# Optimization experiments

Measured on AMD Instinct MI355X. Metric: run time of the kernel, lower is better.

The kernel has to match this reference:

```python
import jax, jax.numpy as jnp
import numpy as np

N, D, DFF, E, F, K, H = 4096, 512, 512, 512, 4096, 1024, 4


def _rn(i, shape, s=0.02):
    return jax.random.normal(jax.random.fold_in(jax.random.key(0), i), shape, dtype=jnp.float32) * s


def setup_inputs():
    inp = {"inputs": jax.random.normal(jax.random.key(1), (N, D), dtype=jnp.float32)}
    i = 10
    for p in ("enc", "dec"):
        for nm, shp in (("wq", (D, D)), ("wk", (D, D)), ("wv", (D, D)), ("wo", (D, D)), ("w1", (D, DFF)), ("w2", (DFF, D))):
            inp[p + "_" + nm] = _rn(i, shp); i += 1
        for nm, shp in (("bq", (D,)), ("bk", (D,)), ("bv", (D,)), ("bo", (D,)), ("b1", (DFF,)), ("b2", (D,))):
            inp[p + "_" + nm] = jnp.zeros(shp, jnp.float32)
        inp[p + "_ln1_g"] = jnp.ones((D,), jnp.float32)
        inp[p + "_ln1_b"] = jnp.zeros((D,), jnp.float32)
        inp[p + "_ln2_g"] = jnp.ones((D,), jnp.float32)
        inp[p + "_ln2_b"] = jnp.zeros((D,), jnp.float32)
    inp["fc1_w"] = _rn(100, (D, E))
    inp["fc1_b"] = jnp.zeros((E,), jnp.float32)
    inp["fc2_w"] = _rn(101, (D, F))
    inp["fc2_b"] = jnp.zeros((F,), jnp.float32)
    inp["emb"] = _rn(102, (K, E), s=0.01)
    return inp


def layer_norm(x, g, b, eps=1e-6):
    mu = jnp.mean(x, axis=-1, keepdims=True)
    var = jnp.mean(jnp.square(x - mu), axis=-1, keepdims=True)
    return (x - mu) * jax.lax.rsqrt(var + eps) * g + b


def row_distance(a, b):
    # cosine similarity between rows (sim in [-1,1]; loss maps (sim+1)/2 -> [0,1])
    an = a * jax.lax.rsqrt(jnp.maximum(jnp.sum(a * a, axis=1, keepdims=True), 1e-12))
    bn = b * jax.lax.rsqrt(jnp.maximum(jnp.sum(b * b, axis=1, keepdims=True), 1e-12))
    return an @ bn.T


def nearest_context(feature, context):
    distances = row_distance(feature, context) * -1.0  # [N, K]
    min_ind = jnp.argmin(distances, axis=1)
    one_hot = jax.nn.one_hot(min_ind, context.shape[0], dtype=jnp.float32)  # [N, K]
    rslt = one_hot @ jax.lax.stop_gradient(context)  # [N, E]
    return rslt, one_hot


@jax.custom_vjp
def vq(feature, context):
    return nearest_context(feature, context)[0]


def _vq_fwd(feature, context):
    value, ind = nearest_context(feature, context)
    return value, ind


def _vq_bwd(ind, d_value):
    # straight-through to feature, scatter-add (via one-hot matmul) to codebook
    return d_value, ind.T @ d_value


vq.defvjp(_vq_fwd, _vq_bwd)


def encoder_layer(x, wq, bq, wk, bk, wv, bv, wo, bo, w1, b1, w2, b2, g1, be1, g2, be2):
    n, d = x.shape
    dh = d // H
    q = (x @ wq + bq).reshape(n, H, dh)
    k = (x @ wk + bk).reshape(n, H, dh)
    v = (x @ wv + bv).reshape(n, H, dh)
    scores = jnp.einsum('nhd,mhd->hnm', q, k) / jnp.sqrt(jnp.float32(dh))
    attn = jax.nn.softmax(scores, axis=-1)
    ctx = jnp.einsum('hnm,mhd->nhd', attn, v).reshape(n, d)
    out1 = layer_norm(x + (ctx @ wo + bo), g1, be1)
    ffn = jax.nn.relu(out1 @ w1 + b1) @ w2 + b2
    return layer_norm(out1 + ffn, g2, be2)


def reference(inputs, enc_wq, enc_wk, enc_wv, enc_wo, enc_w1, enc_w2, enc_bq, enc_bk, enc_bv, enc_bo, enc_b1, enc_b2, enc_ln1_g, enc_ln1_b, enc_ln2_g, enc_ln2_b, dec_wq, dec_wk, dec_wv, dec_wo, dec_w1, dec_w2, dec_bq, dec_bk, dec_bv, dec_bo, dec_b1, dec_b2, dec_ln1_g, dec_ln1_b, dec_ln2_g, dec_ln2_b, fc1_w, fc1_b, fc2_w, fc2_b, emb):
    encoded = encoder_layer(inputs, enc_wq, enc_bq, enc_wk, enc_bk, enc_wv, enc_bv, enc_wo, enc_bo, enc_w1, enc_b1, enc_w2, enc_b2, enc_ln1_g, enc_ln1_b, enc_ln2_g, enc_ln2_b)
    encoded = encoded @ fc1_w + fc1_b  # [N, E]
    vq_feat = vq(encoded, emb)
    _, context_ind = nearest_context(encoded, emb)
    decoded = encoder_layer(vq_feat, dec_wq, dec_bq, dec_wk, dec_bk, dec_wv, dec_bv, dec_wo, dec_bo, dec_w1, dec_b1, dec_w2, dec_b2, dec_ln1_g, dec_ln1_b, dec_ln2_g, dec_ln2_b)
    decoded = jax.nn.relu(decoded @ fc2_w + fc2_b)  # [N, F]
    return encoded, vq_feat, context_ind, decoded, emb
```

## Files before the change

kernel.cpp:

```cpp
#include <hip/hip_runtime.h>
#include <hip/hip_bf16.h>
#include <stdint.h>

typedef __bf16 bf16;
typedef __bf16 bf16x8 __attribute__((ext_vector_type(8)));
typedef float  f32x4v __attribute__((ext_vector_type(4)));

__device__ __forceinline__ void cvt8(const float* v, bf16x8& hh, bf16x8& ll) {
    #pragma unroll
    for (int j = 0; j < 8; j++) {
        bf16 b = (bf16)v[j]; hh[j] = b; ll[j] = (bf16)(v[j] - (float)b);
    }
}

__device__ __forceinline__ float block_reduce_sum256(float v) {
    __shared__ float red[256];
    int tid = threadIdx.x;
    red[tid] = v; __syncthreads();
    #pragma unroll
    for (int s = 128; s > 0; s >>= 1) {
        if (tid < s) red[tid] += red[tid + s];
        __syncthreads();
    }
    float r = red[0]; __syncthreads();
// ... 110 lines not shown
}

template<int BMT, bool RELU>
__global__ __launch_bounds__(256, 2)
void gemm3p(const float* __restrict__ A,
            const bf16* __restrict__ Bph, const bf16* __restrict__ Bpl,
            const float* __restrict__ bias, float* __restrict__ C,
            int K, int lda, int ldb, int ldc)
{
    constexpr int BN = 128, TK = 32;
    constexpr int RM = BMT / 32;
    __shared__ __align__(16) bf16 Ah[BMT * TK];
    __shared__ __align__(16) bf16 Al[BMT * TK];
    __shared__ __align__(16) bf16 Bh[BN * TK];
    __shared__ __align__(16) bf16 Bl[BN * TK];

    const int tid  = threadIdx.x;
    const int wave = tid >> 6, lane = tid & 63;
    const int wr = wave >> 1, wc = wave & 1;
    const long bm = (long)blockIdx.y * BMT;
    const long bn = (long)blockIdx.x * BN;
    const int fr = lane & 15, fq = lane >> 4;

    f32x4v acc[RM][4] = {};

    for (int k0 = 0; k0 < K; k0 += TK) {
        #pragma unroll
        for (int it = 0; it < BMT / 64; it++) {
            const int c = it * 256 + tid;
            const int r = c >> 2, k8 = c & 3;
            const float* src = A + (bm + r) * (long)lda + k0 + k8 * 8;
            float4 f0 = ((const float4*)src)[0], f1 = ((const float4*)src)[1];
            float v[8] = {f0.x, f0.y, f0.z, f0.w, f1.x, f1.y, f1.z, f1.w};
            bf16x8 hh, ll; cvt8(v, hh, ll);
            *(bf16x8*)&Ah[r * TK + k8 * 8] = hh;
            *(bf16x8*)&Al[r * TK + k8 * 8] = ll;
        }
        #pragma unroll
        for (int it = 0; it < 2; it++) {
            const int c = it * 256 + tid;
            const int r = c >> 2, k8 = c & 3;
            const long bo = (bn + r) * (long)ldb + k0 + k8 * 8;
            *(uint4*)&Bh[r * TK + k8 * 8] = *(const uint4*)&Bph[bo];
            *(uint4*)&Bl[r * TK + k8 * 8] = *(const uint4*)&Bpl[bo];
        }
        __syncthreads();

        bf16x8 ah[RM], am[RM], bh[4], bm_[4];
        #pragma unroll
        for (int i = 0; i < RM; i++) {
            const int r = (wr * (BMT / 2) + i * 16 + fr) * TK + fq * 8;
            ah[i] = *(const bf16x8*)&Ah[r];
            am[i] = *(const bf16x8*)&Al[r];
        }
        #pragma unroll
        for (int j = 0; j < 4; j++) {
            const int r = (wc * 64 + j * 16 + fr) * TK + fq * 8;
            bh[j] = *(const bf16x8*)&Bh[r];
            bm_[j] = *(const bf16x8*)&Bl[r];
        }
        #pragma unroll
        for (int i = 0; i < RM; i++)
            #pragma unroll
            for (int j = 0; j < 4; j++) {
                acc[i][j] = __builtin_amdgcn_mfma_f32_16x16x32_bf16(am[i], bh[j], acc[i][j], 0, 0, 0);
                acc[i][j] = __builtin_amdgcn_mfma_f32_16x16x32_bf16(ah[i], bm_[j], acc[i][j], 0, 0, 0);
                acc[i][j] = __builtin_amdgcn_mfma_f32_16x16x32_bf16(ah[i], bh[j], acc[i][j], 0, 0, 0);
            }
        __syncthreads();
    }

    #pragma unroll
    for (int i = 0; i < RM; i++) {
        #pragma unroll
        for (int j = 0; j < 4; j++) {
            const long col = bn + wc * 64 + j * 16 + fr;
            const float bv = bias ? bias[col] : 0.f;
            #pragma unroll
            for (int r = 0; r < 4; r++) {
                const long row = bm + wr * (BMT / 2) + i * 16 + fq * 4 + r;
                float v = acc[i][j][r] + bv;
                if (RELU) v = fmaxf(v, 0.f);
                C[row * (long)ldc + col] = v;
            }
        }
    }
}

__global__ __launch_bounds__(256, 2)
void qkv_gemm(const float* __restrict__ X,
              const float* __restrict__ Wq, const float* __restrict__ Wk, const float* __restrict__ Wv,
              const float* __restrict__ Bq, const float* __restrict__ Bk, const float* __restrict__ Bv,
              float* __restrict__ Qo, bf16* __restrict__ Khi, bf16* __restrict__ Klo,
              bf16* __restrict__ Vthi, bf16* __restrict__ Vtlo)
{
    constexpr int TK = 32, D = 512, N = 4096;
    __shared__ __align__(16) bf16 Ah[64 * TK];
    __shared__ __align__(16) bf16 Al[64 * TK];
    __shared__ __align__(16) bf16 Bh[128 * TK];
    __shared__ __align__(16) bf16 Bl[128 * TK];

    const int tid  = threadIdx.x;
    const int wave = tid >> 6, lane = tid & 63;
    const int wr = wave >> 1, wc = wave & 1;
    const int sel = blockIdx.x >> 2, wcol0 = (blockIdx.x & 3) * 128;
    const long bm = (long)blockIdx.y * 64;
    const int fr = lane & 15, fq = lane >> 4;

    const float* W  = sel == 0 ? Wq : (sel == 1 ? Wk : Wv);
    const float* Bb = sel == 0 ? Bq : (sel == 1 ? Bk : Bv);

    f32x4v acc[2][4] = {};

    for (int k0 = 0; k0 < D; k0 += TK) {
        {
            const int r = tid >> 2, k8 = tid & 3;
            const float* src = X + (bm + r) * (long)D + k0 + k8 * 8;
            float4 f0 = ((const float4*)src)[0], f1 = ((const float4*)src)[1];
            float v[8] = {f0.x, f0.y, f0.z, f0.w, f1.x, f1.y, f1.z, f1.w};
            bf16x8 hh, ll; cvt8(v, hh, ll);
            *(bf16x8*)&Ah[r * TK + k8 * 8] = hh;
            *(bf16x8*)&Al[r * TK + k8 * 8] = ll;
        }
        {
            const int col = tid & 127, bkh = (tid >> 7) * 16;
            const float* src = W + (long)(k0 + bkh) * D + wcol0 + col;
            float v[16];
            #pragma unroll
            for (int kk = 0; kk < 16; kk++) v[kk] = src[(long)kk * D];
            bf16x8 h0, l0, h1, l1; cvt8(v, h0, l0); cvt8(v + 8, h1, l1);
            bf16* hd = &Bh[col * TK + bkh];
            bf16* ld_ = &Bl[col * TK + bkh];
            ((bf16x8*)hd)[0] = h0; ((bf16x8*)hd)[1] = h1;
            ((bf16x8*)ld_)[0] = l0; ((bf16x8*)ld_)[1] = l1;
        }
        __syncthreads();

        bf16x8 ah[2], am[2], bh[4], bm_[4];
        #pragma unroll
        for (int i = 0; i < 2; i++) {
            const int r = (wr * 32 + i * 16 + fr) * TK + fq * 8;
            ah[i] = *(const bf16x8*)&Ah[r];
            am[i] = *(const bf16x8*)&Al[r];
        }
        #pragma unroll
        for (int j = 0; j < 4; j++) {
            const int r = (wc * 64 + j * 16 + fr) * TK + fq * 8;
            bh[j] = *(const bf16x8*)&Bh[r];
            bm_[j] = *(const bf16x8*)&Bl[r];
        }
        #pragma unroll
        for (int i = 0; i < 2; i++)
            #pragma unroll
            for (int j = 0; j < 4; j++) {
                acc[i][j] = __builtin_amdgcn_mfma_f32_16x16x32_bf16(am[i], bh[j], acc[i][j], 0, 0, 0);
                acc[i][j] = __builtin_amdgcn_mfma_f32_16x16x32_bf16(ah[i], bm_[j], acc[i][j], 0, 0, 0);
                acc[i][j] = __builtin_amdgcn_mfma_f32_16x16x32_bf16(ah[i], bh[j], acc[i][j], 0, 0, 0);
            }
        __syncthreads();
    }

    #pragma unroll
    for (int i = 0; i < 2; i++) {
        #pragma unroll
        for (int j = 0; j < 4; j++) {
            const int col = wc * 64 + j * 16 + fr;
// ... 34 lines not shown

    const int tid  = threadIdx.x;
    const int wave = tid >> 6, lane = tid & 63;
    const int wr = wave >> 1, wc = wave & 1;
    const int sel = blockIdx.x >> 2, wcol0 = (blockIdx.x & 3) * 128;
    const long bm = (long)blockIdx.y * 64;
    const int fr = lane & 15, fq = lane >> 4;

    const bf16* Wh = sel == 0 ? Wqh : (sel == 1 ? Wkh : Wvh);
    const bf16* Wl = sel == 0 ? Wql : (sel == 1 ? Wkl : Wvl);
    const float* Bb = sel == 0 ? Bq : (sel == 1 ? Bk : Bv);

    f32x4v acc[2][4] = {};

    for (int k0 = 0; k0 < D; k0 += TK) {
        {
            const int r = tid >> 2, k8 = tid & 3;
            const float* src = X + (bm + r) * (long)D + k0 + k8 * 8;
            float4 f0 = ((const float4*)src)[0], f1 = ((const float4*)src)[1];
            float v[8] = {f0.x, f0.y, f0.z, f0.w, f1.x, f1.y, f1.z, f1.w};
            bf16x8 hh, ll; cvt8(v, hh, ll);
            *(bf16x8*)&Ah[r * TK + k8 * 8] = hh;
            *(bf16x8*)&Al[r * TK + k8 * 8] = ll;
        }
        #pragma unroll
        for (int it = 0; it < 2; it++) {
            const int c = it * 256 + tid;
            const int r = c >> 2, k8 = c & 3;
            const long bo = (long)(wcol0 + r) * D + k0 + k8 * 8;
            *(uint4*)&Bh[r * TK + k8 * 8] = *(const uint4*)&Wh[bo];
            *(uint4*)&Bl[r * TK + k8 * 8] = *(const uint4*)&Wl[bo];
        }
        __syncthreads();

        bf16x8 ah[2], am[2], bh[4], bm_[4];
        #pragma unroll
        for (int i = 0; i < 2; i++) {
            const int r = (wr * 32 + i * 16 + fr) * TK + fq * 8;
            ah[i] = *(const bf16x8*)&Ah[r];
            am[i] = *(const bf16x8*)&Al[r];
        }
        #pragma unroll
        for (int j = 0; j < 4; j++) {
            const int r = (wc * 64 + j * 16 + fr) * TK + fq * 8;
            bh[j] = *(const bf16x8*)&Bh[r];
            bm_[j] = *(const bf16x8*)&Bl[r];
        }
        #pragma unroll
        for (int i = 0; i < 2; i++)
            #pragma unroll
            for (int j = 0; j < 4; j++) {
                acc[i][j] = __builtin_amdgcn_mfma_f32_16x16x32_bf16(am[i], bh[j], acc[i][j], 0, 0, 0);
                acc[i][j] = __builtin_amdgcn_mfma_f32_16x16x32_bf16(ah[i], bm_[j], acc[i][j], 0, 0, 0);
                acc[i][j] = __builtin_amdgcn_mfma_f32_16x16x32_bf16(ah[i], bh[j], acc[i][j], 0, 0, 0);
            }
        __syncthreads();
    }

    #pragma unroll
    for (int i = 0; i < 2; i++) {
        #pragma unroll
        for (int j = 0; j < 4; j++) {
            const int col = wc * 64 + j * 16 + fr;
            const float bv = Bb[wcol0 + col];
            #pragma unroll
            for (int r = 0; r < 4; r++) {
                const long row = bm + wr * 32 + i * 16 + fq * 4 + r;
                const float v = acc[i][j][r] + bv;
                if (sel == 0) {
                    Qo[row * D + wcol0 + col] = v;
                } else {
                    const bf16 hh = (bf16)v;
                    const bf16 ll = (bf16)(v - (float)hh);
                    const long idx = (sel == 1) ? (row * (long)D + wcol0 + col)
                                                : ((long)(wcol0 + col) * N + row);
                    if (sel == 1) { Khi[idx] = hh; Klo[idx] = ll; }
                    else          { Vthi[idx] = hh; Vtlo[idx] = ll; }
                }
            }
        }
    }
}

struct W14 { const float* w[14]; };

__global__ void convert_weights(W14 p, bf16* __restrict__ wsb)
{
    const int z = blockIdx.z;
    const int tid = threadIdx.x;
    int wi, n0, N_;
    if (z < 13) { wi = z; n0 = blockIdx.y * 32; N_ = 512; }
    else        { wi = 13; n0 = (z - 13) * 512 + blockIdx.y * 32; N_ = 4096; }
    const int k0 = blockIdx.x * 32;
    const float* W = p.w[wi];
    const long base = (wi < 13) ? (long)wi * 524288 : 6815744L;
    const long hsz  = (wi < 13) ? 262144L : 2097152L;
    bf16* hi = wsb + base;
    bf16* lo = wsb + base + hsz;

    __shared__ float tile[32][33];
    #pragma unroll
    for (int i = 0; i < 4; i++) {
        const int idx = i * 256 + tid;
        const int r = idx >> 5, c = idx & 31;
        tile[r][c] = W[(long)(k0 + r) * N_ + n0 + c];
    }
    __syncthreads();
    #pragma unroll
    for (int i = 0; i < 4; i++) {
        const int idx = i * 256 + tid;
        const int r = idx >> 5, c = idx & 31;
        const float v = tile[c][r];
        const bf16 h = (bf16)v;
        const long o = (long)(n0 + r) * 512 + k0 + c;
        hi[o] = h;
        lo[o] = (bf16)(v - (float)h);
    }
}

__global__ __launch_bounds__(128, 2)
void flash_attn(const float* __restrict__ Q,
                const bf16* __restrict__ Khi, const bf16* __restrict__ Klo,
                const bf16* __restrict__ Vthi, const bf16* __restrict__ Vtlo,
                float* __restrict__ Op, float* __restrict__ ml)
{
    constexpr int N = 4096, D = 512, SPAN = 1024, TKV = 32, NT = SPAN / TKV;
    constexpr float TS = 0.12751791f;

    __shared__ __align__(16) bf16 smem[16384];
    bf16* Kh = smem;
    bf16* Kl = smem + 4096;
    bf16* Vh = smem + 8192;
    bf16* Vl = smem + 12288;

    const int tid = threadIdx.x;
    const int wave = tid >> 6, lane = tid & 63;
    const int fr = lane & 15, fq = lane >> 4;
    const int qt = blockIdx.x, h = blockIdx.y, s = blockIdx.z;
    const long q0 = (long)qt * 64;

    const int kn = tid >> 4, kk8 = tid & 15;
    const int vd = tid >> 2, vk8 = tid & 3;

    bf16x8 qh[2][4], ql[2][4];
    #pragma unroll
    for (int rg = 0; rg < 2; rg++)
        #pragma unroll
        for (int kt = 0; kt < 4; kt++) {
            const float* src = Q + (q0 + wave * 32 + rg * 16 + fr) * D + h * 128 + kt * 32 + fq * 8;
            float4 f0 = ((const float4*)src)[0], f1 = ((const float4*)src)[1];
            float v[8] = {f0.x, f0.y, f0.z, f0.w, f1.x, f1.y, f1.z, f1.w};
            cvt8(v, qh[rg][kt], ql[rg][kt]);
        }

    f32x4v o[2][8] = {};
    float m_run[2] = {-1e30f, -1e30f}, l_run[2] = {0.f, 0.f};

    const int j0base = s * SPAN;

    #pragma unroll 1
    for (int jt = 0; jt < NT; jt++) {
        const int j0 = j0base + jt * TKV;

        #pragma unroll
        for (int i = 0; i < 4; i++) {
            const int n = kn + 8 * i;
            const long kg = (long)(j0 + n) * D + h * 128 + kk8 * 8;
            const int ko = n * 128 + ((kk8 ^ (n & 15)) << 3);
            *(uint4*)&Kh[ko] = *(const uint4*)&Khi[kg];
            *(uint4*)&Kl[ko] = *(const uint4*)&Klo[kg];
            const int d = vd + 32 * i;
            const long vg = (long)(h * 128 + d) * N + j0 + vk8 * 8;
            const int vo = d * 32 + ((vk8 ^ ((d >> 2) & 3)) << 3);
            *(uint4*)&Vh[vo] = *(const uint4*)&Vthi[vg];
            *(uint4*)&Vl[vo] = *(const uint4*)&Vtlo[vg];
        }
        __syncthreads();

        f32x4v sacc[2][2] = {};
        #pragma unroll
        for (int jb = 0; jb < 2; jb++) {
            bf16x8 kh[4], km[4];
            #pragma unroll
            for (int kt = 0; kt < 4; kt++) {
                const int off = (jb * 16 + fr) * 128 + (((kt * 4 + fq) ^ fr) << 3);
                kh[kt] = *(const bf16x8*)&Kh[off];
                km[kt] = *(const bf16x8*)&Kl[off];
            }
            __builtin_amdgcn_s_setprio(1);
            #pragma unroll
            for (int kt = 0; kt < 4; kt++)
                #pragma unroll
                for (int rg = 0; rg < 2; rg++) {
                    sacc[rg][jb] = __builtin_amdgcn_mfma_f32_16x16x32_bf16(km[kt], qh[rg][kt], sacc[rg][jb], 0, 0, 0);
                    sacc[rg][jb] = __builtin_amdgcn_mfma_f32_16x16x32_bf16(kh[kt], ql[rg][kt], sacc[rg][jb], 0, 0, 0);
                    sacc[rg][jb] = __builtin_amdgcn_mfma_f32_16x16x32_bf16(kh[kt], qh[rg][kt], sacc[rg][jb], 0, 0, 0);
                }
            __builtin_amdgcn_s_setprio(0);
        }

// ... 35 lines not shown
                #pragma unroll
                for (int t2 = 0; t2 < 2; t2++) {
                    const float p0 = p[jb][2 * t2], p1 = p[jb][2 * t2 + 1];
                    const bf16 h0 = (bf16)p0, h1 = (bf16)p1;
                    const unsigned short u0 = __builtin_bit_cast(unsigned short, h0);
                    const unsigned short u1 = __builtin_bit_cast(unsigned short, h1);
                    hp[jb][t2] = (unsigned int)u0 | ((unsigned int)u1 << 16);
                    const bf16 g0 = (bf16)(p0 - (float)h0), g1 = (bf16)(p1 - (float)h1);
                    const unsigned short w0 = __builtin_bit_cast(unsigned short, g0);
                    const unsigned short w1 = __builtin_bit_cast(unsigned short, g1);
                    lp[jb][t2] = (unsigned int)w0 | ((unsigned int)w1 << 16);
                }

            uint4 PH, PL;
            {
                unsigned int phw[4], plw[4];
                #pragma unroll
                for (int w = 0; w < 4; w++) {
                    const int src = ((2 * (fq & 1) + (w >> 1)) << 4) + fr;
                    const unsigned int h0 = (unsigned int)__shfl((int)hp[0][w & 1], src);
                    const unsigned int h1 = (unsigned int)__shfl((int)hp[1][w & 1], src);
                    phw[w] = (fq >> 1) ? h1 : h0;
                    const unsigned int g0 = (unsigned int)__shfl((int)lp[0][w & 1], src);
                    const unsigned int g1 = (unsigned int)__shfl((int)lp[1][w & 1], src);
                    plw[w] = (fq >> 1) ? g1 : g0;
                }
                PH.x = phw[0]; PH.y = phw[1]; PH.z = phw[2]; PH.w = phw[3];
                PL.x = plw[0]; PL.y = plw[1]; PL.z = plw[2]; PL.w = plw[3];
            }
            ph[rg] = __builtin_bit_cast(bf16x8, PH);
            pl[rg] = __builtin_bit_cast(bf16x8, PL);
        }

        #pragma unroll
        for (int rg = 0; rg < 2; rg++) {
            float alr[4];
            #pragma unroll
            for (int r = 0; r < 4; r++) alr[r] = __shfl(alpha[rg], fq * 4 + r);
            #pragma unroll
            for (int jbo = 0; jbo < 8; jbo++)
                #pragma unroll
                for (int r = 0; r < 4; r++)
                    o[rg][jbo][r] *= alr[r];
        }

        #pragma unroll
        for (int jbo = 0; jbo < 8; jbo++) {
            const int off = (jbo * 16 + fr) * 32 + ((fq ^ ((fr >> 2) & 3)) << 3);
            const bf16x8 vh_ = *(const bf16x8*)&Vh[off];
            const bf16x8 vl_ = *(const bf16x8*)&Vl[off];
            __builtin_amdgcn_s_setprio(1);
            #pragma unroll
            for (int rg = 0; rg < 2; rg++) {
                o[rg][jbo] = __builtin_amdgcn_mfma_f32_16x16x32_bf16(pl[rg], vh_, o[rg][jbo], 0, 0, 0);
                o[rg][jbo] = __builtin_amdgcn_mfma_f32_16x16x32_bf16(ph[rg], vl_, o[rg][jbo], 0, 0, 0);
                o[rg][jbo] = __builtin_amdgcn_mfma_f32_16x16x32_bf16(ph[rg], vh_, o[rg][jbo], 0, 0, 0);
            }
            __builtin_amdgcn_s_setprio(0);
        }
        __syncthreads();
    }

    const long sidx = (long)((h * 64 + qt) * 4 + s);
    float* ob = Op + sidx * 8192;
    #pragma unroll
    for (int rg = 0; rg < 2; rg++)
        #pragma unroll
        for (int jbo = 0; jbo < 8; jbo++)
            #pragma unroll
            for (int r = 0; r < 4; r++) {
                const int lrow = wave * 32 + rg * 16 + fq * 4 + r;
                ob[lrow * 128 + jbo * 16 + fr] = o[rg][jbo][r];
            }
    if (fq == 0) {
        #pragma unroll
        for (int rg = 0; rg < 2; rg++) {
            const int lrow = wave * 32 + rg * 16 + fr;
            ml[sidx * 128 + lrow]      = m_run[rg];
            ml[sidx * 128 + 64 + lrow] = l_run[rg];
        }
    }
}

__global__ void flash_merge(const float* __restrict__ Op, const float* __restrict__ ml,
                            float* __restrict__ ctx)
{
    const int idx = blockIdx.x;
    const int h = idx >> 6, qt = idx & 63;
    const int tid = threadIdx.x;
    __shared__ float es[4][64], il[64];
    if (tid < 64) {
        float m[4], l[4];
        #pragma unroll
        for (int s = 0; s < 4; s++) {
            m[s] = ml[(long)(idx * 4 + s) * 128 + tid];
            l[s] = ml[(long)(idx * 4 + s) * 128 + 64 + tid];
        }
        float mx = fmaxf(fmaxf(m[0], m[1]), fmaxf(m[2], m[3]));
        float denom = 0.f;
        #pragma unroll
        for (int s = 0; s < 4; s++) {
            const float e = exp2f(m[s] - mx);
            es[s][tid] = e;
            denom += e * l[s];
        }
        il[tid] = 1.f / denom;
    }
    __syncthreads();
    const long b = (long)idx * 4 * 8192;
    #pragma unroll
    for (int i = 0; i < 32; i++) {
        const int e = tid + i * 256;
        const int row = e >> 7, col = e & 127;
        float v = es[0][row] * Op[b + e] + es[1][row] * Op[b + 8192 + e]
                + es[2][row] * Op[b + 16384 + e] + es[3][row] * Op[b + 24576 + e];
        ctx[(long)(qt * 64 + row) * 512 + h * 128 + col] = v * il[row];
    }
}

__global__ void add_ln_f32(const float* __restrict__ a, const float* __restrict__ b,
                           const float* __restrict__ g, const float* __restrict__ be,
                           float* __restrict__ out)
{
    const long row = blockIdx.x;
    const int tid = threadIdx.x;
    const long base = row * 512L;
    float x0 = a[base + tid]       + b[base + tid];
    float x1 = a[base + tid + 256] + b[base + tid + 256];
    float s = block_reduce_sum256(x0 + x1);
    float mu = s * (1.f / 512.f);
    float d0 = x0 - mu, d1 = x1 - mu;
    float var = block_reduce_sum256(d0 * d0 + d1 * d1) * (1.f / 512.f);
    float invs = rsqrtf(var + 1e-6f);
    out[base + tid]       = d0 * invs * g[tid]       + be[tid];
    out[base + tid + 256] = d1 * invs * g[tid + 256] + be[tid + 256];
}

__global__ void normalize_emb(const float* __restrict__ emb, float* __restrict__ embn)
{
    const long row = blockIdx.x;
    const int tid = threadIdx.x;
    const long base = row * 512L;
    float a0 = emb[base + tid];
    float a1 = emb[base + tid + 256];
    float ss = block_reduce_sum256(a0 * a0 + a1 * a1);
    float sc = rsqrtf(fmaxf(ss, 1e-12f));
    embn[base + tid]       = a0 * sc;
    embn[base + tid + 256] = a1 * sc;
}

__global__ void normalize_emb_p(const float* __restrict__ emb,
                                bf16* __restrict__ hi, bf16* __restrict__ lo)
{
    const long row = blockIdx.x;
    const int tid = threadIdx.x;
    const long base = row * 512L;
    float a0 = emb[base + tid];
    float a1 = emb[base + tid + 256];
    float ss = block_reduce_sum256(a0 * a0 + a1 * a1);
    float sc = rsqrtf(fmaxf(ss, 1e-12f));
    const float e0 = a0 * sc, e1 = a1 * sc;
    const bf16 h0 = (bf16)e0, h1 = (bf16)e1;
    hi[base + tid]       = h0;
    lo[base + tid]       = (bf16)(e0 - (float)h0);
    hi[base + tid + 256] = h1;
    lo[base + tid + 256] = (bf16)(e1 - (float)h1);
}

__global__ void vq_select_onehot(float* __restrict__ sims, const float* __restrict__ emb,
                                 float* __restrict__ vq_out)
{
    __shared__ float sv[256];
    __shared__ int   si[256];
    const long row = blockIdx.x;
    const int tid = threadIdx.x;
    float* s = sims + row * 1024L;
    float v0 = s[tid], v1 = s[tid + 256], v2 = s[tid + 512], v3 = s[tid + 768];
    float best = v0; int bi = tid;
    if (v1 > best) { best = v1; bi = tid + 256; }
    if (v2 > best) { best = v2; bi = tid + 512; }
    if (v3 > best) { best = v3; bi = tid + 768; }
    sv[tid] = best; si[tid] = bi; __syncthreads();
    #pragma unroll
    for (int st = 128; st > 0; st >>= 1) {
        if (tid < st) {
            if (sv[tid + st] > sv[tid] ||
                (sv[tid + st] == sv[tid] && si[tid + st] < si[tid])) {
                sv[tid] = sv[tid + st]; si[tid] = si[tid + st];
            }
        }
        __syncthreads();
    }
    const int idx = si[0];
    s[tid]       = (tid       == idx) ? 1.f : 0.f;
    s[tid + 256] = (tid + 256 == idx) ? 1.f : 0.f;
    s[tid + 512] = (tid + 512 == idx) ? 1.f : 0.f;
    s[tid + 768] = (tid + 768 == idx) ? 1.f : 0.f;
    const float* er = emb + (long)idx * 512;
    float* vr = vq_out + row * 512L;
    vr[tid]       = er[tid];
    vr[tid + 256] = er[tid + 256];
}

struct EncW {
    const float *wq, *wk, *wv, *wo, *w1, *w2;
    const float *bq, *bk, *bv, *bo, *b1, *b2;
    const float *g1, *be1, *g2, *be2;
};

static void run_encoder_g3(hipStream_t stream, const float* x, const EncW& w,
                           float* qb, bf16* khi, bf16* klo, bf16* vthi, bf16* vtlo,
                           float* ctx, float* Op, float* ml,
                           float* x1, float* hb, float* out)
{
    const int N = 4096, D = 512;
    qkv_gemm<<<dim3(12, 64), 256, 0, stream>>>(
        x, w.wq, w.wk, w.wv, w.bq, w.bk, w.bv, qb, khi, klo, vthi, vtlo);
    flash_attn<<<dim3(64, 4, 4), 128, 0, stream>>>(qb, khi, klo, vthi, vtlo, Op, ml);
    flash_merge<<<256, 256, 0, stream>>>(Op, ml, ctx);
    gemm3<64, false, false, true, false><<<dim3(4, 64), 256, 0, stream>>>(
        ctx, w.wo, w.bo, qb, nullptr, nullptr, D, D, D, D, 1.f);
    add_ln_f32<<<N, 256, 0, stream>>>(x, qb, w.g1, w.be1, x1);
    gemm3<64, true, false, true, false><<<dim3(4, 64), 256, 0, stream>>>(
        x1, w.w1, w.b1, hb, nullptr, nullptr, D, D, D, D, 1.f);
    gemm3<64, false, false, true, false><<<dim3(4, 64), 256, 0, stream>>>(
        hb, w.w2, w.b2, qb, nullptr, nullptr, D, D, D, D, 1.f);
    add_ln_f32<<<N, 256, 0, stream>>>(x1, qb, w.g2, w.be2, out);
}

static void run_encoder_g3p(hipStream_t stream, const float* x, const EncW& w,
                            bf16* wsb, int slot0,
                            float* qb, bf16* khi, bf16* klo, bf16* vthi, bf16* vtlo,
                            float* ctx, float* Op, float* ml,
                            float* x1, float* hb, float* out)
{
    const int N = 4096, D = 512;
    auto sh = [&](int i) { return wsb + (long)(slot0 + i) * 524288; };
    auto sl = [&](int i) { return wsb + (long)(slot0 + i) * 524288 + 262144; };
    qkv_gemmp<<<dim3(12, 64), 256, 0, stream>>>(
        x, sh(0), sl(0), sh(1), sl(1), sh(2), sl(2),
        w.bq, w.bk, w.bv, qb, khi, klo, vthi, vtlo);
    flash_attn<<<dim3(64, 4, 4), 128, 0, stream>>>(qb, khi, klo, vthi, vtlo, Op, ml);
    flash_merge<<<256, 256, 0, stream>>>(Op, ml, ctx);
    gemm3p<64, false><<<dim3(4, 64), 256, 0, stream>>>(
        ctx, sh(3), sl(3), w.bo, qb, D, D, D, D);
    add_ln_f32<<<N, 256, 0, stream>>>(x, qb, w.g1, w.be1, x1);
    gemm3p<64, true><<<dim3(4, 64), 256, 0, stream>>>(
        x1, sh(4), sl(4), w.b1, hb, D, D, D, D);
    gemm3p<64, false><<<dim3(4, 64), 256, 0, stream>>>(
        hb, sh(5), sl(5), w.b2, qb, D, D, D, D);
    add_ln_f32<<<N, 256, 0, stream>>>(x1, qb, w.g2, w.be2, out);
}

extern "C" void kernel_launch(void* const* d_in, const int* in_sizes, int n_in,
                              void* d_out, int out_size, void* d_ws, size_t ws_size,
                              hipStream_t stream)
{
    const int N = 4096, D = 512, E = 512, F = 4096, KCB = 1024;
    (void)in_sizes; (void)n_in; (void)out_size;

    const float* x_in  = (const float*)d_in[0];
    const float* fc1_w = (const float*)d_in[33];
    const float* fc1_b = (const float*)d_in[34];
    const float* fc2_w = (const float*)d_in[35];
    const float* fc2_b = (const float*)d_in[36];
    const float* emb   = (const float*)d_in[37];

    float* out0 = (float*)d_out;
    float* out1 = out0 + (size_t)N * E;
    float* out2 = out1 + (size_t)N * E;
    float* out3 = out2 + (size_t)N * KCB;
    float* out4 = out3 + (size_t)N * F;

    char* arena = (char*)out3;
    const size_t MB = 1024 * 1024;
    float* qb     = (float*)(arena + 0 * MB);
    bf16*  khi    = (bf16*) (arena + 8 * MB);
    bf16*  klo    = (bf16*) (arena + 12 * MB);
    bf16*  vthi   = (bf16*) (arena + 16 * MB);
    bf16*  vtlo   = (bf16*) (arena + 20 * MB);
    float* ctx    = (float*)(arena + 24 * MB);
    float* Op     = (float*)(arena + 32 * MB);
    float* decout = (float*)(arena + 56 * MB);
    float* x1     = (float*)(arena + 16 * MB);
    float* hb     = (float*)(arena + 8 * MB);
    float* ml     = (float*)out4;
    float* embn   = out1;
    float* stage  = (float*)out4;

    EncW ew = { (const float*)d_in[1],  (const float*)d_in[2],  (const float*)d_in[3],
                (const float*)d_in[4],  (const float*)d_in[5],  (const float*)d_in[6],
                (const float*)d_in[7],  (const float*)d_in[8],  (const float*)d_in[9],
                (const float*)d_in[10], (const float*)d_in[11], (const float*)d_in[12],
                (const float*)d_in[13], (const float*)d_in[14], (const float*)d_in[15],
                (const float*)d_in[16] };
    EncW dw = { (const float*)d_in[17], (const float*)d_in[18], (const float*)d_in[19],
                (const float*)d_in[20], (const float*)d_in[21], (const float*)d_in[22],
                (const float*)d_in[23], (const float*)d_in[24], (const float*)d_in[25],
                (const float*)d_in[26], (const float*)d_in[27], (const float*)d_in[28],
                (const float*)d_in[29], (const float*)d_in[30], (const float*)d_in[31],
                (const float*)d_in[32] };

    const size_t WS_NEED = 24117248;
    const bool pre = (d_ws != nullptr) && (ws_size >= WS_NEED);

    if (pre) {
        bf16* wsb = (bf16*)d_ws;
        bf16* f2h = wsb + 6815744;  bf16* f2l = f2h + 2097152;
        bf16* enh = wsb + 11010048; bf16* enl = enh + 524288;

        W14 ptrs;
        ptrs.w[0]  = ew.wq; ptrs.w[1]  = ew.wk; ptrs.w[2]  = ew.wv;
        ptrs.w[3]  = ew.wo; ptrs.w[4]  = ew.w1; ptrs.w[5]  = ew.w2;
        ptrs.w[6]  = dw.wq; ptrs.w[7]  = dw.wk; ptrs.w[8]  = dw.wv;
        ptrs.w[9]  = dw.wo; ptrs.w[10] = dw.w1; ptrs.w[11] = dw.w2;
        ptrs.w[12] = fc1_w; ptrs.w[13] = fc2_w;
        convert_weights<<<dim3(16, 16, 21), 256, 0, stream>>>(ptrs, wsb);
        normalize_emb_p<<<KCB, 256, 0, stream>>>(emb, enh, enl);

        run_encoder_g3p(stream, x_in, ew, wsb, 0, qb, khi, klo, vthi, vtlo, ctx, Op, ml, x1, hb, ctx);

        gemm3p<64, false><<<dim3(4, 64), 256, 0, stream>>>(
            ctx, wsb + 12L * 524288, wsb + 12L * 524288 + 262144, fc1_b, out0, D, D, D, E);

        gemm3p<128, false><<<dim3(8, 32), 256, 0, stream>>>(
            out0, enh, enl, nullptr, out2, E, E, E, KCB);
        vq_select_onehot<<<N, 256, 0, stream>>>(out2, emb, out1);

        run_encoder_g3p(stream, out1, dw, wsb, 6, qb, khi, klo, vthi, vtlo, ctx, Op, ml, x1, hb, decout);

        hipMemcpyAsync(stage, decout + (size_t)3584 * D, (size_t)512 * D * sizeof(float),
                       hipMemcpyDeviceToDevice, stream);
        gemm3p<128, true><<<dim3(F / 128, 3584 / 128), 256, 0, stream>>>(
            decout, f2h, f2l, fc2_b, out3, D, D, D, F);
        gemm3p<128, true><<<dim3(F / 128, 512 / 128), 256, 0, stream>>>(
            stage, f2h, f2l, fc2_b, out3 + (size_t)3584 * F, D, D, D, F);

        hipMemcpyAsync(out4, emb, (size_t)KCB * E * sizeof(float), hipMemcpyDeviceToDevice, stream);
    } else {
        normalize_emb<<<KCB, 256, 0, stream>>>(emb, embn);
        run_encoder_g3(stream, x_in, ew, qb, khi, klo, vthi, vtlo, ctx, Op, ml, x1, hb, ctx);
        gemm3<64, false, false, true, false><<<dim3(4, 64), 256, 0, stream>>>(
            ctx, fc1_w, fc1_b, out0, nullptr, nullptr, D, D, E, E, 1.f);
        gemm3<128, false, false, false, false><<<dim3(8, 32), 256, 0, stream>>>(
            out0, embn, nullptr, out2, nullptr, nullptr, E, E, E, KCB, 1.f);
        vq_select_onehot<<<N, 256, 0, stream>>>(out2, emb, out1);
        run_encoder_g3(stream, out1, dw, qb, khi, klo, vthi, vtlo, ctx, Op, ml, x1, hb, decout);
        hipMemcpyAsync(stage, decout + (size_t)3584 * D, (size_t)512 * D * sizeof(float),
                       hipMemcpyDeviceToDevice, stream);
        gemm3<128, true, false, true, false><<<dim3(F / 128, 3584 / 128), 256, 0, stream>>>(
            decout, fc2_w, fc2_b, out3, nullptr, nullptr, D, D, F, F, 1.f);
        gemm3<128, true, false, true, false><<<dim3(F / 128, 512 / 128), 256, 0, stream>>>(
            stage, fc2_w, fc2_b, out3 + (size_t)3584 * F, nullptr, nullptr, D, D, F, F, 1.f);
        hipMemcpyAsync(out4, emb, (size_t)KCB * E * sizeof(float), hipMemcpyDeviceToDevice, stream);
    }
}
```

Before: 822.0 us.

## Emit bf16 hi/lo activation splits in producer epilogues for GEMM consumers

```diff
diff --git a/kernel.cpp b/kernel.cpp
--- a/kernel.cpp
+++ b/kernel.cpp
@@ -216,6 +216,96 @@
                 float v = acc[i][j][r] + bv;
                 if (RELU) v = fmaxf(v, 0.f);
                 C[row * (long)ldc + col] = v;
+            }
+        }
+    }
+}
+
+template<int BMT, bool RELU, bool OUTH>
+__global__ __launch_bounds__(256, 2)
+void gemm3q(const bf16* __restrict__ Agh, const bf16* __restrict__ Agl,
+            const bf16* __restrict__ Bph, const bf16* __restrict__ Bpl,
+            const float* __restrict__ bias, float* __restrict__ C,
+            bf16* __restrict__ Oh, bf16* __restrict__ Ol,
+            int K, int lda, int ldb, int ldc)
+{
+    constexpr int BN = 128, TK = 32;
+    constexpr int RM = BMT / 32;
+    __shared__ __align__(16) bf16 Ah[BMT * TK];
+    __shared__ __align__(16) bf16 Al[BMT * TK];
+    __shared__ __align__(16) bf16 Bh[BN * TK];
+    __shared__ __align__(16) bf16 Bl[BN * TK];
+
+    const int tid  = threadIdx.x;
+    const int wave = tid >> 6, lane = tid & 63;
+    const int wr = wave >> 1, wc = wave & 1;
+    const long bm = (long)blockIdx.y * BMT;
+    const long bn = (long)blockIdx.x * BN;
+    const int fr = lane & 15, fq = lane >> 4;
+
+    f32x4v acc[RM][4] = {};
+
+    for (int k0 = 0; k0 < K; k0 += TK) {
+        #pragma unroll
+        for (int it = 0; it < (BMT + 63) / 64; it++) {
+            const int c = it * 256 + tid;
+            const int r = c >> 2, k8 = c & 3;
+            const long ao = (bm + r) * (long)lda + k0 + k8 * 8;
+            *(uint4*)&Ah[r * TK + k8 * 8] = *(const uint4*)&Agh[ao];
+            *(uint4*)&Al[r * TK + k8 * 8] = *(const uint4*)&Agl[ao];
+        }
+        #pragma unroll
+        for (int it = 0; it < 2; it++) {
+            const int c = it * 256 + tid;
+            const int r = c >> 2, k8 = c & 3;
+            const long bo = (bn + r) * (long)ldb + k0 + k8 * 8;
+            *(uint4*)&Bh[r * TK + k8 * 8] = *(const uint4*)&Bph[bo];
+            *(uint4*)&Bl[r * TK + k8 * 8] = *(const uint4*)&Bpl[bo];
+        }
+        __syncthreads();
+
+        bf16x8 ah[RM], am[RM], bh[4], bm_[4];
+        #pragma unroll
+        for (int i = 0; i < RM; i++) {
+            const int r = (wr * (BMT / 2) + i * 16 + fr) * TK + fq * 8;
+            ah[i] = *(const bf16x8*)&Ah[r];
+            am[i] = *(const bf16x8*)&Al[r];
+        }
+        #pragma unroll
+        for (int j = 0; j < 4; j++) {
+            const int r = (wc * 64 + j * 16 + fr) * TK + fq * 8;
+            bh[j] = *(const bf16x8*)&Bh[r];
+            bm_[j] = *(const bf16x8*)&Bl[r];
+        }
+        #pragma unroll
+        for (int i = 0; i < RM; i++)
+            #pragma unroll
+            for (int j = 0; j < 4; j++) {
+                acc[i][j] = __builtin_amdgcn_mfma_f32_16x16x32_bf16(am[i], bh[j], acc[i][j], 0, 0, 0);
+                acc[i][j] = __builtin_amdgcn_mfma_f32_16x16x32_bf16(ah[i], bm_[j], acc[i][j], 0, 0, 0);
+                acc[i][j] = __builtin_amdgcn_mfma_f32_16x16x32_bf16(ah[i], bh[j], acc[i][j], 0, 0, 0);
+            }
+        __syncthreads();
+    }
+
+    #pragma unroll
+    for (int i = 0; i < RM; i++) {
+        #pragma unroll
+        for (int j = 0; j < 4; j++) {
+            const long col = bn + wc * 64 + j * 16 + fr;
+            const float bv = bias ? bias[col] : 0.f;
+            #pragma unroll
+            for (int r = 0; r < 4; r++) {
+                const long row = bm + wr * (BMT / 2) + i * 16 + fq * 4 + r;
+                float v = acc[i][j][r] + bv;
+                if (RELU) v = fmaxf(v, 0.f);
+                const long idx = row * (long)ldc + col;
+                C[idx] = v;
+                if (OUTH) {
+                    const bf16 hh = (bf16)v;
+                    Oh[idx] = hh;
+                    Ol[idx] = (bf16)(v - (float)hh);
+                }
             }
         }
     }
@@ -416,6 +506,100 @@
     }
 }
 
+__global__ __launch_bounds__(256, 2)
+void qkv_gemmq(const bf16* __restrict__ Xh, const bf16* __restrict__ Xl,
+               const bf16* __restrict__ Wqh, const bf16* __restrict__ Wql,
+               const bf16* __restrict__ Wkh, const bf16* __restrict__ Wkl,
+               const bf16* __restrict__ Wvh, const bf16* __restrict__ Wvl,
+               const float* __restrict__ Bq, const float* __restrict__ Bk, const float* __restrict__ Bv,
+               float* __restrict__ Qo, bf16* __restrict__ Khi, bf16* __restrict__ Klo,
+               bf16* __restrict__ Vthi, bf16* __restrict__ Vtlo)
+{
+    constexpr int TK = 32, D = 512, N = 4096;
+    __shared__ __align__(16) bf16 Ah[64 * TK];
+    __shared__ __align__(16) bf16 Al[64 * TK];
+    __shared__ __align__(16) bf16 Bh[128 * TK];
+    __shared__ __align__(16) bf16 Bl[128 * TK];
+
+    const int tid  = threadIdx.x;
+    const int wave = tid >> 6, lane = tid & 63;
+    const int wr = wave >> 1, wc = wave & 1;
+    const int sel = blockIdx.x >> 2, wcol0 = (blockIdx.x & 3) * 128;
+    const long bm = (long)blockIdx.y * 64;
+    const int fr = lane & 15, fq = lane >> 4;
+
+    const bf16* Wh = sel == 0 ? Wqh : (sel == 1 ? Wkh : Wvh);
+    const bf16* Wl = sel == 0 ? Wql : (sel == 1 ? Wkl : Wvl);
+    const float* Bb = sel == 0 ? Bq : (sel == 1 ? Bk : Bv);
+
+    f32x4v acc[2][4] = {};
+
+    for (int k0 = 0; k0 < D; k0 += TK) {
+        {
+            const int r = tid >> 2, k8 = tid & 3;
+            const long ao = (bm + r) * (long)D + k0 + k8 * 8;
+            *(uint4*)&Ah[r * TK + k8 * 8] = *(const uint4*)&Xh[ao];
+            *(uint4*)&Al[r * TK + k8 * 8] = *(const uint4*)&Xl[ao];
+        }
+        #pragma unroll
+        for (int it = 0; it < 2; it++) {
+            const int c = it * 256 + tid;
+            const int r = c >> 2, k8 = c & 3;
+            const long bo = (long)(wcol0 + r) * D + k0 + k8 * 8;
+            *(uint4*)&Bh[r * TK + k8 * 8] = *(const uint4*)&Wh[bo];
+            *(uint4*)&Bl[r * TK + k8 * 8] = *(const uint4*)&Wl[bo];
+        }
+        __syncthreads();
+
+        bf16x8 ah[2], am[2], bh[4], bm_[4];
+        #pragma unroll
+        for (int i = 0; i < 2; i++) {
+            const int r = (wr * 32 + i * 16 + fr) * TK + fq * 8;
+            ah[i] = *(const bf16x8*)&Ah[r];
+            am[i] = *(const bf16x8*)&Al[r];
+        }
+        #pragma unroll
+        for (int j = 0; j < 4; j++) {
+            const int r = (wc * 64 + j * 16 + fr) * TK + fq * 8;
+            bh[j] = *(const bf16x8*)&Bh[r];
+            bm_[j] = *(const bf16x8*)&Bl[r];
+        }
+        #pragma unroll
+        for (int i = 0; i < 2; i++)
+            #pragma unroll
+            for (int j = 0; j < 4; j++) {
+                acc[i][j] = __builtin_amdgcn_mfma_f32_16x16x32_bf16(am[i], bh[j], acc[i][j], 0, 0, 0);
+                acc[i][j] = __builtin_amdgcn_mfma_f32_16x16x32_bf16(ah[i], bm_[j], acc[i][j], 0, 0, 0);
+                acc[i][j] = __builtin_amdgcn_mfma_f32_16x16x32_bf16(ah[i], bh[j], acc[i][j], 0, 0, 0);
+            }
+        __syncthreads();
+    }
+
+    #pragma unroll
+    for (int i = 0; i < 2; i++) {
+        #pragma unroll
+        for (int j = 0; j < 4; j++) {
+            const int col = wc * 64 + j * 16 + fr;
+            const float bv = Bb[wcol0 + col];
+            #pragma unroll
+            for (int r = 0; r < 4; r++) {
+                const long row = bm + wr * 32 + i * 16 + fq * 4 + r;
+                const float v = acc[i][j][r] + bv;
+                if (sel == 0) {
+                    Qo[row * D + wcol0 + col] = v;
+                } else {
+                    const bf16 hh = (bf16)v;
+                    const bf16 ll = (bf16)(v - (float)hh);
+                    const long idx = (sel == 1) ? (row * (long)D + wcol0 + col)
+                                                : ((long)(wcol0 + col) * N + row);
+                    if (sel == 1) { Khi[idx] = hh; Klo[idx] = ll; }
+                    else          { Vthi[idx] = hh; Vtlo[idx] = ll; }
+                }
+            }
+        }
+    }
+}
+
 struct W14 { const float* w[14]; };
 
 __global__ void convert_weights(W14 p, bf16* __restrict__ wsb)
@@ -450,6 +634,17 @@
         hi[o] = h;
         lo[o] = (bf16)(v - (float)h);
     }
+}
+
+__global__ void convert_x(const float* __restrict__ x,
+                          bf16* __restrict__ hi, bf16* __restrict__ lo)
+{
+    const long i = ((long)blockIdx.x * 256 + threadIdx.x) * 8;
+    float4 f0 = ((const float4*)(x + i))[0], f1 = ((const float4*)(x + i))[1];
+    float v[8] = {f0.x, f0.y, f0.z, f0.w, f1.x, f1.y, f1.z, f1.w};
+    bf16x8 hh, ll; cvt8(v, hh, ll);
+    *(bf16x8*)&hi[i] = hh;
+    *(bf16x8*)&lo[i] = ll;
 }
 
 __global__ __launch_bounds__(128, 2)
@@ -651,8 +846,9 @@
     }
 }
 
-__global__ void flash_merge(const float* __restrict__ Op, const float* __restrict__ ml,
-                            float* __restrict__ ctx)
+template<bool OUTH>
+__global__ void flash_merge_t(const float* __restrict__ Op, const float* __restrict__ ml,
+                              float* __restrict__ ctx, bf16* __restrict__ ch, bf16* __restrict__ cl)
 {
     const int idx = blockIdx.x;
     const int h = idx >> 6, qt = idx & 63;
@@ -683,13 +879,21 @@
         const int row = e >> 7, col = e & 127;
         float v = es[0][row] * Op[b + e] + es[1][row] * Op[b + 8192 + e]
                 + es[2][row] * Op[b + 16384 + e] + es[3][row] * Op[b + 24576 + e];
-        ctx[(long)(qt * 64 + row) * 512 + h * 128 + col] = v * il[row];
-    }
-}
-
-__global__ void add_ln_f32(const float* __restrict__ a, const float* __restrict__ b,
-                           const float* __restrict__ g, const float* __restrict__ be,
-                           float* __restrict__ out)
+        const float vv = v * il[row];
+        const long cidx = (long)(qt * 64 + row) * 512 + h * 128 + col;
+        ctx[cidx] = vv;
+        if (OUTH) {
+            const bf16 hh = (bf16)vv;
+            ch[cidx] = hh;
+            cl[cidx] = (bf16)(vv - (float)hh);
+        }
+    }
+}
+
+template<bool OUTH>
+__global__ void add_ln_t(const float* __restrict__ a, const float* __restrict__ b,
+                         const float* __restrict__ g, const float* __restrict__ be,
+                         float* __restrict__ out, bf16* __restrict__ oh, bf16* __restrict__ ol)
 {
     const long row = blockIdx.x;
     const int tid = threadIdx.x;
@@ -701,8 +905,17 @@
     float d0 = x0 - mu, d1 = x1 - mu;
     float var = block_reduce_sum256(d0 * d0 + d1 * d1) * (1.f / 512.f);
     float invs = rsqrtf(var + 1e-6f);
-    out[base + tid]       = d0 * invs * g[tid]       + be[tid];
-    out[base + tid + 256] = d1 * invs * g[tid + 256] + be[tid + 256];
+    const float y0 = d0 * invs * g[tid]       + be[tid];
+    const float y1 = d1 * invs * g[tid + 256] + be[tid + 256];
+    out[base + tid]       = y0;
+    out[base + tid + 256] = y1;
+    if (OUTH) {
+        const bf16 h0 = (bf16)y0, h1 = (bf16)y1;
+        oh[base + tid]       = h0;
+        ol[base + tid]       = (bf16)(y0 - (float)h0);
+        oh[base + tid + 256] = h1;
+        ol[base + tid + 256] = (bf16)(y1 - (float)h1);
+    }
 }
 
 __global__ void normalize_emb(const float* __restrict__ emb, float* __restrict__ embn)
@@ -736,8 +949,9 @@
     lo[base + tid + 256] = (bf16)(e1 - (float)h1);
 }
 
-__global__ void vq_select_onehot(float* __restrict__ sims, const float* __restrict__ emb,
-                                 float* __restrict__ vq_out)
+template<bool OUTH>
+__global__ void vq_select_t(float* __restrict__ sims, const float* __restrict__ emb,
+                            float* __restrict__ vq_out, bf16* __restrict__ vh, bf16* __restrict__ vl)
 {
     __shared__ float sv[256];
     __shared__ int   si[256];
@@ -767,8 +981,16 @@
     s[tid + 768] = (tid + 768 == idx) ? 1.f : 0.f;
     const float* er = emb + (long)idx * 512;
     float* vr = vq_out + row * 512L;
-    vr[tid]       = er[tid];
-    vr[tid + 256] = er[tid + 256];
+    const float e0 = er[tid], e1 = er[tid + 256];
+    vr[tid]       = e0;
+    vr[tid + 256] = e1;
+    if (OUTH) {
+        const bf16 h0 = (bf16)e0, h1 = (bf16)e1;
+        vh[row * 512 + tid]       = h0;
+        vl[row * 512 + tid]       = (bf16)(e0 - (float)h0);
+        vh[row * 512 + tid + 256] = h1;
+        vl[row * 512 + tid + 256] = (bf16)(e1 - (float)h1);
+    }
 }
 
 struct EncW {
@@ -786,15 +1008,15 @@
     qkv_gemm<<<dim3(12, 64), 256, 0, stream>>>(
         x, w.wq, w.wk, w.wv, w.bq, w.bk, w.bv, qb, khi, klo, vthi, vtlo);
     flash_attn<<<dim3(64, 4, 4), 128, 0, stream>>>(qb, khi, klo, vthi, vtlo, Op, ml);
-    flash_merge<<<256, 256, 0, stream>>>(Op, ml, ctx);
+    flash_merge_t<false><<<256, 256, 0, stream>>>(Op, ml, ctx, nullptr, nullptr);
     gemm3<64, false, false, true, false><<<dim3(4, 64), 256, 0, stream>>>(
         ctx, w.wo, w.bo, qb, nullptr, nullptr, D, D, D, D, 1.f);
-    add_ln_f32<<<N, 256, 0, stream>>>(x, qb, w.g1, w.be1, x1);
+    add_ln_t<false><<<N, 256, 0, stream>>>(x, qb, w.g1, w.be1, x1, nullptr, nullptr);
     gemm3<64, true, false, true, false><<<dim3(4, 64), 256, 0, stream>>>(
         x1, w.w1, w.b1, hb, nullptr, nullptr, D, D, D, D, 1.f);
     gemm3<64, false, false, true, false><<<dim3(4, 64), 256, 0, stream>>>(
         hb, w.w2, w.b2, qb, nullptr, nullptr, D, D, D, D, 1.f);
-    add_ln_f32<<<N, 256, 0, stream>>>(x1, qb, w.g2, w.be2, out);
+    add_ln_t<false><<<N, 256, 0, stream>>>(x1, qb, w.g2, w.be2, out, nullptr, nullptr);
 }
 
 static void run_encoder_g3p(hipStream_t stream, const float* x, const EncW& w,
@@ -810,15 +1032,43 @@
         x, sh(0), sl(0), sh(1), sl(1), sh(2), sl(2),
         w.bq, w.bk, w.bv, qb, khi, klo, vthi, vtlo);
     flash_attn<<<dim3(64, 4, 4), 128, 0, stream>>>(qb, khi, klo, vthi, vtlo, Op, ml);
-    flash_merge<<<256, 256, 0, stream>>>(Op, ml, ctx);
+    flash_merge_t<false><<<256, 256, 0, stream>>>(Op, ml, ctx, nullptr, nullptr);
     gemm3p<64, false><<<dim3(4, 64), 256, 0, stream>>>(
         ctx, sh(3), sl(3), w.bo, qb, D, D, D, D);
-    add_ln_f32<<<N, 256, 0, stream>>>(x, qb, w.g1, w.be1, x1);
+    add_ln_t<false><<<N, 256, 0, stream>>>(x, qb, w.g1, w.be1, x1, nullptr, nullptr);
     gemm3p<64, true><<<dim3(4, 64), 256, 0, stream>>>(
         x1, sh(4), sl(4), w.b1, hb, D, D, D, D);
     gemm3p<64, false><<<dim3(4, 64), 256, 0, stream>>>(
         hb, sh(5), sl(5), w.b2, qb, D, D, D, D);
-    add_ln_f32<<<N, 256, 0, stream>>>(x1, qb, w.g2, w.be2, out);
+    add_ln_t<false><<<N, 256, 0, stream>>>(x1, qb, w.g2, w.be2, out, nullptr, nullptr);
+}
+
+static void run_encoder_g3q(hipStream_t stream,
+                            const float* xres,
+                            const bf16* xah, const bf16* xal,
+                            const EncW& w, bf16* wsb, int slot0,
+                            bf16* ctxh, bf16* ctxl, bf16* x1h, bf16* x1l,
+                            bf16* hbh, bf16* hbl, bf16* o2h, bf16* o2l,
+                            float* qb, bf16* khi, bf16* klo, bf16* vthi, bf16* vtlo,
+                            float* ctx, float* Op, float* ml,
+                            float* x1, float* hb, float* out)
+{
+    const int N = 4096, D = 512;
+    auto sh = [&](int i) { return wsb + (long)(slot0 + i) * 524288; };
+    auto sl = [&](int i) { return wsb + (long)(slot0 + i) * 524288 + 262144; };
+    qkv_gemmq<<<dim3(12, 64), 256, 0, stream>>>(
+        xah, xal, sh(0), sl(0), sh(1), sl(1), sh(2), sl(2),
+        w.bq, w.bk, w.bv, qb, khi, klo, vthi, vtlo);
+    flash_attn<<<dim3(64, 4, 4), 128, 0, stream>>>(qb, khi, klo, vthi, vtlo, Op, ml);
+    flash_merge_t<true><<<256, 256, 0, stream>>>(Op, ml, ctx, ctxh, ctxl);
+    gemm3q<64, false, false><<<dim3(4, 64), 256, 0, stream>>>(
+        ctxh, ctxl, sh(3), sl(3), w.bo, qb, nullptr, nullptr, D, D, D, D);
+    add_ln_t<true><<<N, 256, 0, stream>>>(xres, qb, w.g1, w.be1, x1, x1h, x1l);
+    gemm3q<64, true, true><<<dim3(4, 64), 256, 0, stream>>>(
+        x1h, x1l, sh(4), sl(4), w.b1, hb, hbh, hbl, D, D, D, D);
+    gemm3q<64, false, false><<<dim3(4, 64), 256, 0, stream>>>(
+        hbh, hbl, sh(5), sl(5), w.b2, qb, nullptr, nullptr, D, D, D, D);
+    add_ln_t<true><<<N, 256, 0, stream>>>(x1, qb, w.g2, w.be2, out, o2h, o2l);
 }
 
 extern "C" void kernel_launch(void* const* d_in, const int* in_sizes, int n_in,
@@ -870,10 +1120,12 @@
                 (const float*)d_in[29], (const float*)d_in[30], (const float*)d_in[31],
                 (const float*)d_in[32] };
 
-    const size_t WS_NEED = 24117248;
-    const bool pre = (d_ws != nullptr) && (ws_size >= WS_NEED);
-
-    if (pre) {
+    const size_t WS_NEED1 = 24117248;
+    const size_t WS_NEED2 = 74448896;
+    const bool pre2 = (d_ws != nullptr) && (ws_size >= WS_NEED2);
+    const bool pre1 = !pre2 && (d_ws != nullptr) && (ws_size >= WS_NEED1);
+
+    if (pre2 || pre1) {
         bf16* wsb = (bf16*)d_ws;
         bf16* f2h = wsb + 6815744;  bf16* f2l = f2h + 2097152;
         bf16* enh = wsb + 11010048; bf16* enl = enh + 524288;
@@ -887,25 +1139,50 @@
         convert_weights<<<dim3(16, 16, 21), 256, 0, stream>>>(ptrs, wsb);
         normalize_emb_p<<<KCB, 256, 0, stream>>>(emb, enh, enl);
 
-        run_encoder_g3p(stream, x_in, ew, wsb, 0, qb, khi, klo, vthi, vtlo, ctx, Op, ml, x1, hb, ctx);
-
-        gemm3p<64, false><<<dim3(4, 64), 256, 0, stream>>>(
-            ctx, wsb + 12L * 524288, wsb + 12L * 524288 + 262144, fc1_b, out0, D, D, D, E);
-
-        gemm3p<128, false><<<dim3(8, 32), 256, 0, stream>>>(
-            out0, enh, enl, nullptr, out2, E, E, E, KCB);
-        vq_select_onehot<<<N, 256, 0, stream>>>(out2, emb, out1);
-
-        run_encoder_g3p(stream, out1, dw, wsb, 6, qb, khi, klo, vthi, vtlo, ctx, Op, ml, x1, hb, decout);
-
-        hipMemcpyAsync(stage, decout + (size_t)3584 * D, (size_t)512 * D * sizeof(float),
-                       hipMemcpyDeviceToDevice, stream);
-        gemm3p<128, true><<<dim3(F / 128, 3584 / 128), 256, 0, stream>>>(
-            decout, f2h, f2l, fc2_b, out3, D, D, D, F);
-        gemm3p<128, true><<<dim3(F / 128, 512 / 128), 256, 0, stream>>>(
-            stage, f2h, f2l, fc2_b, out3 + (size_t)3584 * F, D, D, D, F);
-
-        hipMemcpyAsync(out4, emb, (size_t)KCB * E * sizeof(float), hipMemcpyDeviceToDevice, stream);
+        if (pre2) {
+            auto AH = [&](int s_) { return wsb + 12058624L + (long)s_ * 4194304; };
+            auto AL = [&](int s_) { return wsb + 12058624L + (long)s_ * 4194304 + 2097152; };
+            bf16 *xah = AH(0), *xal = AL(0);
+            bf16 *cth = AH(1), *ctl = AL(1);
+            bf16 *x1h = AH(2), *x1l = AL(2);
+            bf16 *hbh = AH(3), *hbl = AL(3);
+            bf16 *o2h = AH(4), *o2l = AL(4);
+            bf16 *f1h = AH(5), *f1l = AL(5);
+
+            convert_x<<<1024, 256, 0, stream>>>(x_in, xah, xal);
+
+            run_encoder_g3q(stream, x_in, xah, xal, ew, wsb, 0,
+                            cth, ctl, x1h, x1l, hbh, hbl, o2h, o2l,
+                            qb, khi, klo, vthi, vtlo, ctx, Op, ml, x1, hb, ctx);
+            gemm3q<64, false, true><<<dim3(4, 64), 256, 0, stream>>>(
+                o2h, o2l, wsb + 12L * 524288, wsb + 12L * 524288 + 262144,
+                fc1_b, out0, f1h, f1l, D, D, D, E);
+            gemm3q<128, false, false><<<dim3(8, 32), 256, 0, stream>>>(
+                f1h, f1l, enh, enl, nullptr, out2, nullptr, nullptr, E, E, E, KCB);
+            vq_select_t<true><<<N, 256, 0, stream>>>(out2, emb, out1, xah, xal);
+            run_encoder_g3q(stream, out1, xah, xal, dw, wsb, 6,
+                            cth, ctl, x1h, x1l, hbh, hbl, o2h, o2l,
+                            qb, khi, klo, vthi, vtlo, ctx, Op, ml, x1, hb, decout);
+            gemm3q<128, true, false><<<dim3(F / 128, N / 128), 256, 0, stream>>>(
+                o2h, o2l, f2h, f2l, fc2_b, out3, nullptr, nullptr, D, D, D, F);
+
+            hipMemcpyAsync(out4, emb, (size_t)KCB * E * sizeof(float), hipMemcpyDeviceToDevice, stream);
+        } else {
+            run_encoder_g3p(stream, x_in, ew, wsb, 0, qb, khi, klo, vthi, vtlo, ctx, Op, ml, x1, hb, ctx);
+            gemm3p<64, false><<<dim3(4, 64), 256, 0, stream>>>(
+                ctx, wsb + 12L * 524288, wsb + 12L * 524288 + 262144, fc1_b, out0, D, D, D, E);
+            gemm3p<128, false><<<dim3(8, 32), 256, 0, stream>>>(
+                out0, enh, enl, nullptr, out2, E, E, E, KCB);
+            vq_select_t<false><<<N, 256, 0, stream>>>(out2, emb, out1, nullptr, nullptr);
+            run_encoder_g3p(stream, out1, dw, wsb, 6, qb, khi, klo, vthi, vtlo, ctx, Op, ml, x1, hb, decout);
+            hipMemcpyAsync(stage, decout + (size_t)3584 * D, (size_t)512 * D * sizeof(float),
+                           hipMemcpyDeviceToDevice, stream);
+            gemm3p<128, true><<<dim3(F / 128, 3584 / 128), 256, 0, stream>>>(
+                decout, f2h, f2l, fc2_b, out3, D, D, D, F);
+            gemm3p<128, true><<<dim3(F / 128, 512 / 128), 256, 0, stream>>>(
+                stage, f2h, f2l, fc2_b, out3 + (size_t)3584 * F, D, D, D, F);
+            hipMemcpyAsync(out4, emb, (size_t)KCB * E * sizeof(float), hipMemcpyDeviceToDevice, stream);
+        }
     } else {
         normalize_emb<<<KCB, 256, 0, stream>>>(emb, embn);
         run_encoder_g3(stream, x_in, ew, qb, khi, klo, vthi, vtlo, ctx, Op, ml, x1, hb, ctx);
@@ -913,7 +1190,7 @@
             ctx, fc1_w, fc1_b, out0, nullptr, nullptr, D, D, E, E, 1.f);
         gemm3<128, false, false, false, false><<<dim3(8, 32), 256, 0, stream>>>(
             out0, embn, nullptr, out2, nullptr, nullptr, E, E, E, KCB, 1.f);
-        vq_select_onehot<<<N, 256, 0, stream>>>(out2, emb, out1);
+        vq_select_t<false><<<N, 256, 0, stream>>>(out2, emb, out1, nullptr, nullptr);
         run_encoder_g3(stream, out1, dw, qb, khi, klo, vthi, vtlo, ctx, Op, ml, x1, hb, decout);
         hipMemcpyAsync(stage, decout + (size_t)3584 * D, (size_t)512 * D * sizeof(float),
                        hipMemcpyDeviceToDevice, stream);
```

New measurement: 800.6 us. 1.03x faster.
